# Kernel optimization log

Measured on AMD Instinct MI355X. Metric: run time of the kernel, lower is better.

Reference implementation:

```python
import jax, jax.numpy as jnp
import numpy as np

B, N, CT = 64, 256, 3
HID, HEADS = 256, 4
C = HID // HEADS          # per-head channels
E = 8192                  # number of edges
NEG = 0.2                 # GATv2 leaky_relu negative slope
EPS_BN = 1e-5


def setup_inputs() -> dict:
    key = jax.random.key(0)
    ks = jax.random.split(key, 32)
    F_in = N * CT
    s1 = 1.0 / np.sqrt(F_in)
    sh = 1.0 / np.sqrt(HID)
    inp = {
        "x": jax.random.normal(ks[0], (B, N, N, CT), jnp.float32),
        "edge_index": jax.random.randint(ks[1], (2, E), 0, N, dtype=jnp.int32),
        # node_proj: Linear + BatchNorm1d (eval) params
        "W1": jax.random.normal(ks[2], (F_in, HID), jnp.float32) * s1,
        "b1": jnp.zeros((HID,), jnp.float32),
        "g1": jnp.ones((HID,), jnp.float32),
        "be1": jnp.zeros((HID,), jnp.float32),
        "m1": jnp.zeros((HID,), jnp.float32),
        "v1": jnp.ones((HID,), jnp.float32),
        # GATv2 layer 0
        "Wl0": jax.random.normal(ks[3], (HID, HID), jnp.float32) * sh,
        "bl0": jnp.zeros((HID,), jnp.float32),
        "Wr0": jax.random.normal(ks[4], (HID, HID), jnp.float32) * sh,
        "br0": jnp.zeros((HID,), jnp.float32),
        "att0": jax.random.normal(ks[5], (HEADS, C), jnp.float32) * (1.0 / np.sqrt(C)),
        "bo0": jnp.zeros((HID,), jnp.float32),
        # GATv2 layer 1
        "Wl1": jax.random.normal(ks[6], (HID, HID), jnp.float32) * sh,
        "bl1": jnp.zeros((HID,), jnp.float32),
        "Wr1": jax.random.normal(ks[7], (HID, HID), jnp.float32) * sh,
        "br1": jnp.zeros((HID,), jnp.float32),
        "att1": jax.random.normal(ks[8], (HEADS, C), jnp.float32) * (1.0 / np.sqrt(C)),
        "bo1": jnp.zeros((HID,), jnp.float32),
        # output_proj: Linear + BatchNorm1d (eval) params
        "W2": jax.random.normal(ks[9], (HID, HID), jnp.float32) * sh,
        "b2": jnp.zeros((HID,), jnp.float32),
        "g2": jnp.ones((HID,), jnp.float32),
        "be2": jnp.zeros((HID,), jnp.float32),
        "m2": jnp.zeros((HID,), jnp.float32),
        "v2": jnp.ones((HID,), jnp.float32),
    }
    return inp


def _bn(x, g, b, m, v):
    # BatchNorm1d in eval mode: per-feature affine with running stats
    return (x - m) * jax.lax.rsqrt(v + EPS_BN) * g + b


def _gatv2(h, src, dst, Wl, bl, Wr, br, att, bo):
    # h: (N, HID). GATv2Conv (PyG semantics): lin_l on source, lin_r on target.
    xl = (h @ Wl + bl).reshape(N, HEADS, C)
    xr = (h @ Wr + br).reshape(N, HEADS, C)
    x_j = xl[src]                        # (E, H, C) source features
    x_i = xr[dst]                        # (E, H, C) target features
    e = jax.nn.leaky_relu(x_i + x_j, NEG)
    logits = jnp.einsum('ehc,hc->eh', e, att)          # (E, H)
    mx = jax.ops.segment_max(logits, dst, num_segments=N)
    a = jnp.exp(logits - mx[dst])
    den = jax.ops.segment_sum(a, dst, num_segments=N)
    a = a / (den[dst] + 1e-16)                         # neighborhood softmax
    out = jax.ops.segment_sum(x_j * a[:, :, None], dst, num_segments=N)
    return out.reshape(N, HID) + bo


def reference(x, edge_index, W1, b1, g1, be1, m1, v1,
              Wl0, bl0, Wr0, br0, att0, bo0,
              Wl1, bl1, Wr1, br1, att1, bo1,
              W2, b2, g2, be2, m2, v2):
    gelu = lambda t: jax.nn.gelu(t, approximate=False)
    xf = x.reshape(B, N, N * CT)
    # node_proj (eval: dropout off, BN uses running stats -> vmappable)
    h = gelu(_bn(xf @ W1 + b1, g1, be1, m1, v1))       # (B, N, HID)
    src, dst = edge_index[0], edge_index[1]

    def per_sample(hn):
        h0 = gelu(_gatv2(hn, src, dst, Wl0, bl0, Wr0, br0, att0, bo0))
        h1 = gelu(_gatv2(h0, src, dst, Wl1, bl1, Wr1, br1, att1, bo1))
        return h1.mean(axis=0)                          # mean over nodes

    pooled = jax.vmap(per_sample)(h)                    # (B, HID)
    return gelu(_bn(pooled @ W2 + b2, g2, be2, m2, v2))
```

## Files before the change

### kernel.cpp

```cpp
#include <hip/hip_runtime.h>
#include <hip/hip_bf16.h>
#include <math.h>

#define BATCH   64
#define NNODES  256
#define HID     256
#define HEADS   4
#define CDIM    64
#define NEDGES  8192
#define NEG_SLOPE 0.2f
#define EPS_BN 1e-5f


typedef __bf16 bf16_t;
typedef __bf16 bf16x8 __attribute__((ext_vector_type(8)));
typedef float  f32x4  __attribute__((ext_vector_type(4)));

__device__ __forceinline__ float gelu_f(float x) {
    return 0.5f * x * (1.0f + erff(x * 0.70710678118654752440f));
}

#define SWZ(r, c) ((c) ^ ((r) & 3) ^ (((r) >> 2) & 3) ^ (((r) >> 4) & 3))

__global__ __launch_bounds__(256) void prep_kernel(
        const int* __restrict__ ei,
        const float* __restrict__ W1, const float* __restrict__ Wa,
        const float* __restrict__ Wb, const float* __restrict__ Wc,
        const float* __restrict__ Wd,
        int* __restrict__ noff, int* __restrict__ csrc,
        bf16_t* __restrict__ T1, bf16_t* __restrict__ Ta,
        bf16_t* __restrict__ Tb, bf16_t* __restrict__ Tc,
        bf16_t* __restrict__ Td) {
    const int bx = blockIdx.x;
    const int tid = threadIdx.x;
    if (bx == 448) {
        __shared__ int cnt[NNODES];
        __shared__ int off_s[NNODES + 1];
        cnt[tid] = 0;
        __syncthreads();
        for (int e = tid; e < NEDGES; e += 256) atomicAdd(&cnt[ei[NEDGES + e]], 1);
        __syncthreads();
        if (tid == 0) {
            int s = 0;
            for (int i = 0; i < NNODES; ++i) { off_s[i] = s; s += cnt[i]; }
            off_s[NNODES] = s;
        }
        __syncthreads();
        cnt[tid] = off_s[tid];
        noff[tid] = off_s[tid];
        if (tid == 0) noff[NNODES] = off_s[NNODES];
        __syncthreads();
        for (int e = tid; e < NEDGES; e += 256) {
            int d = ei[NEDGES + e];
            int p = atomicAdd(&cnt[d], 1);
            csrc[p] = ei[e];
        }
        return;
    }
    __shared__ float tile[32][33];
    const float* in; bf16_t* out; int t;
    if (bx < 192) { in = W1; out = T1; t = bx; }
    else {
        int r = bx - 192, mid = r >> 6; t = r & 63;
        if (mid == 0) { in = Wa; out = Ta; }
        else if (mid == 1) { in = Wb; out = Tb; }
        else if (mid == 2) { in = Wc; out = Tc; }
        else { in = Wd; out = Td; }
    }
    const int kt = t >> 3, nt = t & 7;
    const int k0 = kt * 32, n0 = nt * 32;
    const int x = tid & 31, y = tid >> 5;
    #pragma unroll
    for (int j = 0; j < 4; ++j)
        tile[y + j * 8][x] = in[(size_t)(k0 + y + j * 8) * 256 + n0 + x];
    __syncthreads();
    #pragma unroll
    for (int j = 0; j < 4; ++j) {
        const int n = n0 + y + j * 8;
        out[((size_t)kt * 256 + n) * 32 + x] = (bf16_t)tile[x][y + j * 8];
    }
}

template<int A_F32, int DUAL, int EPI_BN, int PERM>
__global__ __launch_bounds__(256, 4) void gemm_kernel(
        const void* __restrict__ Ap,
        const bf16_t* __restrict__ Bt0, const bf16_t* __restrict__ Bt1,
        bf16_t* __restrict__ C0p, bf16_t* __restrict__ C1p, int K,
        const float* __restrict__ bias0, const float* __restrict__ bias1,
        const float* __restrict__ g, const float* __restrict__ be,
        const float* __restrict__ mu, const float* __restrict__ var) {
    __shared__ bf16_t As[32 * 32];
    __shared__ bf16_t Bs[256 * 32];
    const int tid  = threadIdx.x;
    const int lane = tid & 63;
    const int wv   = tid >> 6;
    const int mblk = blockIdx.y * 32;
    const bool second = DUAL && (blockIdx.x == 1);
    const bf16_t* Bt = second ? Bt1 : Bt0;
    bf16_t* Cp = second ? C1p : C0p;
    const float* bias = second ? bias1 : bias0;

    f32x4 acc[2][4];
    #pragma unroll
    for (int f = 0; f < 2; ++f)
        #pragma unroll
        for (int t = 0; t < 4; ++t) acc[f][t] = (f32x4){0.f, 0.f, 0.f, 0.f};

    const int arow = tid >> 2;
    const int achk = tid & 3;
    const int gr   = mblk + arow;
    const int arr  = PERM ? ((gr & 63) * 256 + (gr >> 6)) : gr;
    const int fm   = lane & 15, q = lane >> 4;

    for (int k0 = 0; k0 < K; k0 += 32) {
        if (tid < 128) {
            bf16x8 v;
            if (A_F32) {
                const float* ap = (const float*)Ap + (size_t)arr * K + k0 + achk * 8;
                f32x4 a0 = *(const f32x4*)ap;
                f32x4 a1 = *(const f32x4*)(ap + 4);
                #pragma unroll
                for (int j = 0; j < 4; ++j) { v[j] = (bf16_t)a0[j]; v[4 + j] = (bf16_t)a1[j]; }
            } else {
                v = *(const bf16x8*)((const bf16_t*)Ap + (size_t)arr * K + k0 + achk * 8);
            }
            *(bf16x8*)(&As[(arow * 4 + SWZ(arow, achk)) * 8]) = v;
        }
        {
            const bf16_t* panel = Bt + (size_t)(k0 >> 5) * (256 * 32);
            #pragma unroll
            for (int c = 0; c < 4; ++c) {
                const int f = c * 256 + tid;
                const bf16x8 bv = *(const bf16x8*)(panel + (size_t)f * 8);
                const int n = f >> 2, kc = f & 3;
                *(bf16x8*)(&Bs[(n * 4 + SWZ(n, kc)) * 8]) = bv;
            }
        }
        __syncthreads();

        bf16x8 af[2], bfv[4];
        #pragma unroll
        for (int f = 0; f < 2; ++f) {
            const int r = f * 16 + fm;
            af[f] = *(const bf16x8*)(&As[(r * 4 + SWZ(r, q)) * 8]);
        }
        #pragma unroll
        for (int t = 0; t < 4; ++t) {
            const int n = wv * 64 + t * 16 + fm;
            bfv[t] = *(const bf16x8*)(&Bs[(n * 4 + SWZ(n, q)) * 8]);
        }
        #pragma unroll
        for (int f = 0; f < 2; ++f)
            #pragma unroll
            for (int t = 0; t < 4; ++t)
                acc[f][t] = __builtin_amdgcn_mfma_f32_16x16x32_bf16(
                    af[f], bfv[t], acc[f][t], 0, 0, 0);
        __syncthreads();
    }

    const int quad = lane >> 4, cn = lane & 15;
    #pragma unroll
    for (int t = 0; t < 4; ++t) {
        const int n = wv * 64 + t * 16 + cn;
        const float bv = bias[n];
        float scale = 1.0f, shift = 0.0f;
        if (EPI_BN) {
            float s = g[n] * rsqrtf(var[n] + EPS_BN);
            scale = s;
            shift = be[n] - mu[n] * s;
        }
        #pragma unroll
        for (int f = 0; f < 2; ++f) {
            #pragma unroll
            for (int r = 0; r < 4; ++r) {
                const int m = mblk + f * 16 + quad * 4 + r;
                float val = acc[f][t][r] + bv;
                if (EPI_BN) val = gelu_f(val * scale + shift);
                Cp[(size_t)m * 256 + n] = (bf16_t)val;
            }
        }
    }
}

__global__ __launch_bounds__(256) void edge_kernel(
        const bf16_t* __restrict__ XL, const bf16_t* __restrict__ XR,
        const float* __restrict__ att, const float* __restrict__ bo,
        const int* __restrict__ noff, const int* __restrict__ csrc,
        bf16_t* __restrict__ Hout) {
    const int bid  = blockIdx.x;
    const int i    = bid >> 3;
    const int tid  = threadIdx.x;
    const int w    = tid >> 6;
    const int lane = tid & 63;
    const int bg   = lane >> 3;
    const int cg   = lane & 7;
    const int b    = (bid & 7) * 8 + bg;
    const int cbase = w * CDIM + cg * 8;
    const size_t orow = ((size_t)i * BATCH + b) * HID + cbase;
    const float* bor = bo + cbase;

    const int s0 = noff[i], s1 = noff[i + 1];
    if (s0 == s1) {
        bf16x8 ov;
        #pragma unroll
        for (int q = 0; q < 8; ++q) ov[q] = (bf16_t)gelu_f(bor[q]);
        *(bf16x8*)(Hout + orow) = ov;
        return;
    }

    float a6[8], a4[8], xi[8];
    {
        const float* ar = att + cbase;
        const bf16x8 xr = *(const bf16x8*)(XR + orow);
        #pragma unroll
        for (int q = 0; q < 8; ++q) {
            float a = ar[q];
            a6[q] = 0.6f * a; a4[q] = 0.4f * a;
            xi[q] = (float)xr[q];
        }
    }

    const bf16_t* XLb = XL + (size_t)b * HID + cbase;
    const size_t RSTR = (size_t)BATCH * HID;

    float mA = -1e30f, dA = 0.f, mB = -1e30f, dB = 0.f;
    float accA[8], accB[8];
    #pragma unroll
    for (int q = 0; q < 8; ++q) { accA[q] = 0.f; accB[q] = 0.f; }

    int jA = csrc[s0];
    int jB = csrc[(s0 + 1 < s1) ? s0 + 1 : s0];
    bf16x8 xA = *(const bf16x8*)(XLb + (size_t)jA * RSTR);
    bf16x8 xB = *(const bf16x8*)(XLb + (size_t)jB * RSTR);

    for (int e = s0; e < s1; e += 2) {
        const int nA = (e + 2 < s1) ? e + 2 : s0;
        const int nB = (e + 3 < s1) ? e + 3 : s0;
        const int jnA = csrc[nA], jnB = csrc[nB];
        const bf16x8 xnA = *(const bf16x8*)(XLb + (size_t)jnA * RSTR);
        const bf16x8 xnB = *(const bf16x8*)(XLb + (size_t)jnB * RSTR);

        float fA[8], fB[8];
        #pragma unroll
        for (int q = 0; q < 8; ++q) { fA[q] = (float)xA[q]; fB[q] = (float)xB[q]; }
        float pA = 0.f, pB = 0.f;
        #pragma unroll
        for (int q = 0; q < 8; ++q) {
            const float zA = xi[q] + fA[q];
            const float zB = xi[q] + fB[q];
            pA = fmaf(a6[q], zA, pA);
            pB = fmaf(a6[q], zB, pB);
            pA = fmaf(a4[q], __builtin_fabsf(zA), pA);
            pB = fmaf(a4[q], __builtin_fabsf(zB), pB);
        }
        pA += __shfl_xor(pA, 1, 64);  pB += __shfl_xor(pB, 1, 64);
        pA += __shfl_xor(pA, 2, 64);  pB += __shfl_xor(pB, 2, 64);
        pA += __shfl_xor(pA, 4, 64);  pB += __shfl_xor(pB, 4, 64);

        const float mnA = fmaxf(mA, pA);
        const float alA = __expf(mA - mnA);
        const float wA  = __expf(pA - mnA);
        const float vB  = (e + 1 < s1) ? 1.f : 0.f;
        const float mnB = fmaxf(mB, pB);
        const float alB = __expf(mB - mnB);
        const float wB  = __expf(pB - mnB) * vB;
        dA = dA * alA + wA;
        dB = dB * alB + wB;
        #pragma unroll
        for (int q = 0; q < 8; ++q) {
            accA[q] = fmaf(accA[q], alA, wA * fA[q]);
            accB[q] = fmaf(accB[q], alB, wB * fB[q]);
        }
        mA = mnA; mB = mnB;
        xA = xnA; xB = xnB;
    }

    const float mm = fmaxf(mA, mB);
    const float g1 = __expf(mA - mm);
    const float g2 = __expf(mB - mm);
    const float inv = 1.0f / (dA * g1 + dB * g2 + 1e-16f);
    bf16x8 ov;
    #pragma unroll
    for (int q = 0; q < 8; ++q) {
        const float o = (accA[q] * g1 + accB[q] * g2) * inv + bor[q];
        ov[q] = (bf16_t)gelu_f(o);
    }
    *(bf16x8*)(Hout + orow) = ov;
}

__global__ __launch_bounds__(256) void pf_kernel(
        const bf16_t* __restrict__ H1, const float* __restrict__ W2,
        const float* __restrict__ b2, const float* __restrict__ g2,
        const float* __restrict__ be2, const float* __restrict__ m2,
        const float* __restrict__ v2, float* __restrict__ out) {
    __shared__ float pl[HID];
    const int b = blockIdx.x, f = threadIdx.x;
    float s = 0.f;
    for (int n = 0; n < NNODES; ++n)
        s += (float)H1[((size_t)n * BATCH + b) * HID + f];
    pl[f] = s * (1.0f / (float)NNODES);
    __syncthreads();
    float acc = 0.f;
    for (int k = 0; k < HID; ++k) acc += pl[k] * W2[(size_t)k * HID + f];
    acc += b2[f];
    const float scale = g2[f] * rsqrtf(v2[f] + EPS_BN);
    acc = (acc - m2[f]) * scale + be2[f];
    out[b * HID + f] = gelu_f(acc);
}

extern "C" void kernel_launch(void* const* d_in, const int* in_sizes, int n_in,
                              void* d_out, int out_size, void* d_ws, size_t ws_size,
                              hipStream_t stream) {
    const float* x    = (const float*)d_in[0];
    const int*   ei   = (const int*)d_in[1];
    const float* W1   = (const float*)d_in[2];
    const float* b1   = (const float*)d_in[3];
    const float* g1   = (const float*)d_in[4];
    const float* be1  = (const float*)d_in[5];
    const float* m1   = (const float*)d_in[6];
    const float* v1   = (const float*)d_in[7];
    const float* Wl0  = (const float*)d_in[8];
    const float* bl0  = (const float*)d_in[9];
    const float* Wr0  = (const float*)d_in[10];
    const float* br0  = (const float*)d_in[11];
    const float* att0 = (const float*)d_in[12];
    const float* bo0  = (const float*)d_in[13];
    const float* Wl1  = (const float*)d_in[14];
    const float* bl1  = (const float*)d_in[15];
    const float* Wr1  = (const float*)d_in[16];
    const float* br1  = (const float*)d_in[17];
    const float* att1 = (const float*)d_in[18];
    const float* bo1  = (const float*)d_in[19];
    const float* W2   = (const float*)d_in[20];
    const float* b2   = (const float*)d_in[21];
    const float* g2   = (const float*)d_in[22];
    const float* be2  = (const float*)d_in[23];
    const float* m2   = (const float*)d_in[24];
    const float* v2   = (const float*)d_in[25];

    char* ws = (char*)d_ws;
    const int M = BATCH * NNODES;
    const size_t SZ_BF = (size_t)M * HID * sizeof(bf16_t);

    int*    noff = (int*)ws;                ws += 2048;
    int*    csrc = (int*)ws;                ws += 32768;
    bf16_t* W1t  = (bf16_t*)ws;             ws += 256 * 768 * 2;
    bf16_t* Wl0t = (bf16_t*)ws;             ws += 256 * 256 * 2;
    bf16_t* Wr0t = (bf16_t*)ws;             ws += 256 * 256 * 2;
    bf16_t* Wl1t = (bf16_t*)ws;             ws += 256 * 256 * 2;
    bf16_t* Wr1t = (bf16_t*)ws;             ws += 256 * 256 * 2;
    bf16_t* H    = (bf16_t*)ws;             ws += SZ_BF;
    bf16_t* H2   = (bf16_t*)ws;             ws += SZ_BF;
    bf16_t* XL   = (bf16_t*)ws;             ws += SZ_BF;
    bf16_t* XR   = (bf16_t*)ws;             ws += SZ_BF;

    prep_kernel<<<449, 256, 0, stream>>>(ei, W1, Wl0, Wr0, Wl1, Wr1,
                                         noff, csrc, W1t, Wl0t, Wr0t, Wl1t, Wr1t);

    gemm_kernel<1, 0, 1, 1><<<dim3(1, 512), 256, 0, stream>>>(
        x, W1t, nullptr, H, nullptr, 768, b1, nullptr, g1, be1, m1, v1);

    gemm_kernel<0, 1, 0, 0><<<dim3(2, 512), 256, 0, stream>>>(
        H, Wl0t, Wr0t, XL, XR, 256, bl0, br0, nullptr, nullptr, nullptr, nullptr);
    edge_kernel<<<NNODES * 8, 256, 0, stream>>>(XL, XR, att0, bo0, noff, csrc, H2);

    gemm_kernel<0, 1, 0, 0><<<dim3(2, 512), 256, 0, stream>>>(
        H2, Wl1t, Wr1t, XL, XR, 256, bl1, br1, nullptr, nullptr, nullptr, nullptr);
    edge_kernel<<<NNODES * 8, 256, 0, stream>>>(XL, XR, att1, bo1, noff, csrc, H);

    pf_kernel<<<BATCH, 256, 0, stream>>>(H, W2, b2, g2, be2, m2, v2, (float*)d_out);
}
```

Baseline: 297.1 us.

## Double-buffer GEMM tiles with register prefetch, parallel CSR scan, split pooling

The GEMM now keeps two shared-memory buffers and holds the next K-tile in registers while the current tile runs through the MFMAs, which removes one barrier per iteration and hides global load latency. K becomes a template parameter so the K loop can be fully unrolled. The CSR offset build swaps a serial single-thread prefix sum for a parallel Hillis-Steele scan. Mean pooling is split across four node chunks per sample in a separate kernel, adding one launch and a small scratch buffer but giving more parallelism than the old 64-block pooling loop. The extra registers and doubled LDS may lower occupancy under launch_bounds(256,4).

```diff
diff --git a/kernel.cpp b/kernel.cpp
--- a/kernel.cpp
+++ b/kernel.cpp
@@ -35,20 +35,24 @@
     const int tid = threadIdx.x;
     if (bx == 448) {
         __shared__ int cnt[NNODES];
-        __shared__ int off_s[NNODES + 1];
+        __shared__ int sc[NNODES];
         cnt[tid] = 0;
         __syncthreads();
         for (int e = tid; e < NEDGES; e += 256) atomicAdd(&cnt[ei[NEDGES + e]], 1);
         __syncthreads();
-        if (tid == 0) {
-            int s = 0;
-            for (int i = 0; i < NNODES; ++i) { off_s[i] = s; s += cnt[i]; }
-            off_s[NNODES] = s;
-        }
+        sc[tid] = cnt[tid];
         __syncthreads();
-        cnt[tid] = off_s[tid];
-        noff[tid] = off_s[tid];
-        if (tid == 0) noff[NNODES] = off_s[NNODES];
+        #pragma unroll
+        for (int ofs = 1; ofs < 256; ofs <<= 1) {
+            const int t = (tid >= ofs) ? sc[tid - ofs] : 0;
+            __syncthreads();
+            sc[tid] += t;
+            __syncthreads();
+        }
+        const int excl = sc[tid] - cnt[tid];
+        noff[tid] = excl;
+        if (tid == 255) noff[NNODES] = sc[255];
+        cnt[tid] = excl;
         __syncthreads();
         for (int e = tid; e < NEDGES; e += 256) {
             int d = ei[NEDGES + e];
@@ -81,16 +85,17 @@
     }
 }
 
-template<int A_F32, int DUAL, int EPI_BN, int PERM>
+template<int A_F32, int DUAL, int EPI_BN, int PERM, int KTILES>
 __global__ __launch_bounds__(256, 4) void gemm_kernel(
         const void* __restrict__ Ap,
         const bf16_t* __restrict__ Bt0, const bf16_t* __restrict__ Bt1,
-        bf16_t* __restrict__ C0p, bf16_t* __restrict__ C1p, int K,
+        bf16_t* __restrict__ C0p, bf16_t* __restrict__ C1p,
         const float* __restrict__ bias0, const float* __restrict__ bias1,
         const float* __restrict__ g, const float* __restrict__ be,
         const float* __restrict__ mu, const float* __restrict__ var) {
-    __shared__ bf16_t As[32 * 32];
-    __shared__ bf16_t Bs[256 * 32];
+    __shared__ bf16_t As[2][32 * 32];
+    __shared__ bf16_t Bs[2][256 * 32];
+    const int K = KTILES * 32;
     const int tid  = threadIdx.x;
     const int lane = tid & 63;
     const int wv   = tid >> 6;
@@ -106,48 +111,70 @@
         #pragma unroll
         for (int t = 0; t < 4; ++t) acc[f][t] = (f32x4){0.f, 0.f, 0.f, 0.f};
 
-    const int arow = tid >> 2;
+    const int arow = (tid & 127) >> 2;
     const int achk = tid & 3;
     const int gr   = mblk + arow;
     const int arr  = PERM ? ((gr & 63) * 256 + (gr >> 6)) : gr;
     const int fm   = lane & 15, q = lane >> 4;
-
-    for (int k0 = 0; k0 < K; k0 += 32) {
+    const int bn   = tid >> 2;
+
+    f32x4 a0, a1; bf16x8 aReg; bf16x8 bReg[4];
+
+    if (tid < 128) {
+        if (A_F32) {
+            const float* ap = (const float*)Ap + (size_t)arr * K + achk * 8;
+            a0 = *(const f32x4*)ap; a1 = *(const f32x4*)(ap + 4);
+        } else {
+            aReg = *(const bf16x8*)((const bf16_t*)Ap + (size_t)arr * K + achk * 8);
+        }
+    }
+    {
+        const bf16_t* panel = Bt + (size_t)tid * 8;
+        #pragma unroll
+        for (int c = 0; c < 4; ++c) bReg[c] = *(const bf16x8*)(panel + c * 2048);
+    }
+
+    #pragma unroll
+    for (int kt = 0; kt < KTILES; ++kt) {
+        const int buf = kt & 1;
         if (tid < 128) {
             bf16x8 v;
             if (A_F32) {
-                const float* ap = (const float*)Ap + (size_t)arr * K + k0 + achk * 8;
-                f32x4 a0 = *(const f32x4*)ap;
-                f32x4 a1 = *(const f32x4*)(ap + 4);
                 #pragma unroll
                 for (int j = 0; j < 4; ++j) { v[j] = (bf16_t)a0[j]; v[4 + j] = (bf16_t)a1[j]; }
-            } else {
-                v = *(const bf16x8*)((const bf16_t*)Ap + (size_t)arr * K + k0 + achk * 8);
+            } else v = aReg;
+            *(bf16x8*)(&As[buf][(arow * 4 + SWZ(arow, achk)) * 8]) = v;
+        }
+        #pragma unroll
+        for (int c = 0; c < 4; ++c) {
+            const int n = c * 64 + bn;
+            *(bf16x8*)(&Bs[buf][(n * 4 + SWZ(n, achk)) * 8]) = bReg[c];
+        }
+        __syncthreads();
+        if (kt + 1 < KTILES) {
+            const int k0 = (kt + 1) * 32;
+            if (tid < 128) {
+                if (A_F32) {
+                    const float* ap = (const float*)Ap + (size_t)arr * K + k0 + achk * 8;
+                    a0 = *(const f32x4*)ap; a1 = *(const f32x4*)(ap + 4);
+                } else {
+                    aReg = *(const bf16x8*)((const bf16_t*)Ap + (size_t)arr * K + k0 + achk * 8);
+                }
             }
-            *(bf16x8*)(&As[(arow * 4 + SWZ(arow, achk)) * 8]) = v;
-        }
-        {
-            const bf16_t* panel = Bt + (size_t)(k0 >> 5) * (256 * 32);
+            const bf16_t* panel = Bt + (size_t)(kt + 1) * (256 * 32) + (size_t)tid * 8;
             #pragma unroll
-            for (int c = 0; c < 4; ++c) {
-                const int f = c * 256 + tid;
-                const bf16x8 bv = *(const bf16x8*)(panel + (size_t)f * 8);
-                const int n = f >> 2, kc = f & 3;
-                *(bf16x8*)(&Bs[(n * 4 + SWZ(n, kc)) * 8]) = bv;
-            }
-        }
-        __syncthreads();
-
+            for (int c = 0; c < 4; ++c) bReg[c] = *(const bf16x8*)(panel + c * 2048);
+        }
         bf16x8 af[2], bfv[4];
         #pragma unroll
         for (int f = 0; f < 2; ++f) {
             const int r = f * 16 + fm;
-            af[f] = *(const bf16x8*)(&As[(r * 4 + SWZ(r, q)) * 8]);
+            af[f] = *(const bf16x8*)(&As[buf][(r * 4 + SWZ(r, q)) * 8]);
         }
         #pragma unroll
         for (int t = 0; t < 4; ++t) {
             const int n = wv * 64 + t * 16 + fm;
-            bfv[t] = *(const bf16x8*)(&Bs[(n * 4 + SWZ(n, q)) * 8]);
+            bfv[t] = *(const bf16x8*)(&Bs[buf][(n * 4 + SWZ(n, q)) * 8]);
         }
         #pragma unroll
         for (int f = 0; f < 2; ++f)
@@ -155,7 +182,6 @@
             for (int t = 0; t < 4; ++t)
                 acc[f][t] = __builtin_amdgcn_mfma_f32_16x16x32_bf16(
                     af[f], bfv[t], acc[f][t], 0, 0, 0);
-        __syncthreads();
     }
 
     const int quad = lane >> 4, cn = lane & 15;
@@ -288,24 +314,33 @@
     *(bf16x8*)(Hout + orow) = ov;
 }
 
-__global__ __launch_bounds__(256) void pf_kernel(
-        const bf16_t* __restrict__ H1, const float* __restrict__ W2,
+__global__ __launch_bounds__(256) void pool_kernel(const bf16_t* __restrict__ H1,
+                                                   float* __restrict__ P) {
+    const int b = blockIdx.x, c = blockIdx.y, f = threadIdx.x;
+    const bf16_t* p = H1 + ((size_t)(c * 64) * BATCH + b) * HID + f;
+    float s = 0.f;
+    for (int n = 0; n < 64; ++n) s += (float)p[(size_t)n * BATCH * HID];
+    P[((size_t)b * 4 + c) * HID + f] = s;
+}
+
+__global__ __launch_bounds__(256) void final_kernel(
+        const float* __restrict__ P, const float* __restrict__ W2,
         const float* __restrict__ b2, const float* __restrict__ g2,
         const float* __restrict__ be2, const float* __restrict__ m2,
         const float* __restrict__ v2, float* __restrict__ out) {
     __shared__ float pl[HID];
     const int b = blockIdx.x, f = threadIdx.x;
+    float s4 = 0.f;
+    #pragma unroll
+    for (int c = 0; c < 4; ++c) s4 += P[((size_t)b * 4 + c) * HID + f];
+    pl[f] = s4 * (1.0f / (float)NNODES);
+    __syncthreads();
     float s = 0.f;
-    for (int n = 0; n < NNODES; ++n)
-        s += (float)H1[((size_t)n * BATCH + b) * HID + f];
-    pl[f] = s * (1.0f / (float)NNODES);
-    __syncthreads();
-    float acc = 0.f;
-    for (int k = 0; k < HID; ++k) acc += pl[k] * W2[(size_t)k * HID + f];
-    acc += b2[f];
+    for (int k = 0; k < HID; ++k) s += pl[k] * W2[(size_t)k * HID + f];
+    s += b2[f];
     const float scale = g2[f] * rsqrtf(v2[f] + EPS_BN);
-    acc = (acc - m2[f]) * scale + be2[f];
-    out[b * HID + f] = gelu_f(acc);
+    s = (s - m2[f]) * scale + be2[f];
+    out[b * HID + f] = gelu_f(s);
 }
 
 extern "C" void kernel_launch(void* const* d_in, const int* in_sizes, int n_in,
@@ -353,20 +388,23 @@
     bf16_t* H2   = (bf16_t*)ws;             ws += SZ_BF;
     bf16_t* XL   = (bf16_t*)ws;             ws += SZ_BF;
     bf16_t* XR   = (bf16_t*)ws;             ws += SZ_BF;
+    float*  P    = (float*)ws;              ws += BATCH * 4 * HID * 4;
 
     prep_kernel<<<449, 256, 0, stream>>>(ei, W1, Wl0, Wr0, Wl1, Wr1,
                                          noff, csrc, W1t, Wl0t, Wr0t, Wl1t, Wr1t);
 
-    gemm_kernel<1, 0, 1, 1><<<dim3(1, 512), 256, 0, stream>>>(
-        x, W1t, nullptr, H, nullptr, 768, b1, nullptr, g1, be1, m1, v1);
-
-    gemm_kernel<0, 1, 0, 0><<<dim3(2, 512), 256, 0, stream>>>(
-        H, Wl0t, Wr0t, XL, XR, 256, bl0, br0, nullptr, nullptr, nullptr, nullptr);
+    gemm_kernel<1, 0, 1, 1, 24><<<dim3(1, 512), 256, 0, stream>>>(
+        x, W1t, nullptr, H, nullptr, b1, nullptr, g1, be1, m1, v1);
+
+    gemm_kernel<0, 1, 0, 0, 8><<<dim3(2, 512), 256, 0, stream>>>(
+        H, Wl0t, Wr0t, XL, XR, bl0, br0, nullptr, nullptr, nullptr, nullptr);
     edge_kernel<<<NNODES * 8, 256, 0, stream>>>(XL, XR, att0, bo0, noff, csrc, H2);
 
-    gemm_kernel<0, 1, 0, 0><<<dim3(2, 512), 256, 0, stream>>>(
-        H2, Wl1t, Wr1t, XL, XR, 256, bl1, br1, nullptr, nullptr, nullptr, nullptr);
+    gemm_kernel<0, 1, 0, 0, 8><<<dim3(2, 512), 256, 0, stream>>>(
+        H2, Wl1t, Wr1t, XL, XR, bl1, br1, nullptr, nullptr, nullptr, nullptr);
     edge_kernel<<<NNODES * 8, 256, 0, stream>>>(XL, XR, att1, bo1, noff, csrc, H);
 
-    pf_kernel<<<BATCH, 256, 0, stream>>>(H, W2, b2, g2, be2, m2, v2, (float*)d_out);
-}
+    pool_kernel<<<dim3(BATCH, 4), 256, 0, stream>>>(H, P);
+    final_kernel<<<BATCH, 256, 0, stream>>>(P, W2, b2, g2, be2, m2, v2,
+                                            (float*)d_out);
+}
```

Measured after the change: 278.8 us. 1.07x faster.
